# Optimization experiments

Measured on AMD Instinct MI355X. Metric: run time of the kernel, lower is better.

## Reference

```python
import jax, jax.numpy as jnp
import numpy as np

HIDDEN = 7168
NH = 32
DQ = 1536
DKV = 512
DH = 128   # up_projected_head_size
DR = 64    # rope_head_size
ROPE_BASE = 10000.0


def rms_norm(x, g):
    eps = jnp.finfo(x.dtype).eps
    var = jnp.mean(x * x, axis=-1, keepdims=True)
    return x * jax.lax.rsqrt(var + eps) * g


def apply_rope(x):
    # x: [B, H, S, D] -- rotate-half RoPE with cos/sin built as cat(freqs,freqs)
    S, D = x.shape[-2], x.shape[-1]
    inv_freq = 1.0 / (ROPE_BASE ** (jnp.arange(0, D, 2, dtype=jnp.float32) / D))
    t = jnp.arange(S, dtype=jnp.float32)
    freqs = jnp.outer(t, inv_freq)                 # [S, D/2]
    emb = jnp.concatenate([freqs, freqs], axis=-1)  # [S, D]
    cos, sin = jnp.cos(emb), jnp.sin(emb)
    x1, x2 = x[..., : D // 2], x[..., D // 2:]
    rotated = jnp.concatenate([-x2, x1], axis=-1)
    return x * cos + rotated * sin


def setup_inputs() -> dict:
    key = jax.random.key(0)
    ks = jax.random.split(key, 8)
    s = 0.02
    return {
        "hidden_states": jax.random.normal(ks[0], (1, 2048, HIDDEN), jnp.float32),
        "W_dq": jax.random.normal(ks[1], (HIDDEN, DQ), jnp.float32) * s,
        "g_q": jnp.ones((DQ,), jnp.float32),
        "W_uq": jax.random.normal(ks[2], (DQ, NH * (DH + DR)), jnp.float32) * s,
        "W_dkv": jax.random.normal(ks[3], (HIDDEN, DKV + DR), jnp.float32) * s,
        "g_kv": jnp.ones((DKV,), jnp.float32),
        "W_ukv": jax.random.normal(ks[4], (DKV, NH * 2 * DH), jnp.float32) * s,
        "W_o": jax.random.normal(ks[5], (NH * DH, HIDDEN), jnp.float32) * s,
    }


def reference(hidden_states, W_dq, g_q, W_uq, W_dkv, g_kv, W_ukv, W_o):
    B, S, _ = hidden_states.shape
    # Q path: down-proj -> RMSNorm -> up-proj -> split nope/rope parts
    c_q = hidden_states @ W_dq                                   # [B,S,DQ]
    qcr = (rms_norm(c_q, g_q) @ W_uq).reshape(B, S, NH, DH + DR)
    qcr = qcr.transpose(0, 2, 1, 3)                              # [B,NH,S,DH+DR]
    q_c, q_r = qcr[..., :DH], qcr[..., DH:]
    # KV path: joint down-proj for compressed latent + shared MQA rope key
    ckv_kr = hidden_states @ W_dkv                               # [B,S,DKV+DR]
    c_kv, k_r = ckv_kr[..., :DKV], ckv_kr[..., DKV:]
    k_r = k_r[:, None, :, :]                                     # [B,1,S,DR]
    kv = (rms_norm(c_kv, g_kv) @ W_ukv).reshape(B, S, NH, 2 * DH)
    kv = kv.transpose(0, 2, 1, 3)                                # [B,NH,S,2*DH]
    k_c, v = kv[..., :DH], kv[..., DH:]
    # partial RoPE
    q_r = apply_rope(q_r)
    k_r = apply_rope(k_r)
    q = jnp.concatenate([q_c, q_r], axis=-1)                     # [B,NH,S,DH+DR]
    k = jnp.concatenate([k_c, jnp.broadcast_to(k_r, (B, NH, S, DR))], axis=-1)
    # non-causal SDPA, scale = 1/sqrt(q head dim)
    scale = 1.0 / np.sqrt(DH + DR)
    scores = jnp.einsum("bhqd,bhkd->bhqk", q, k) * scale
    attn = jax.nn.softmax(scores, axis=-1)
    o = jnp.einsum("bhqk,bhkd->bhqd", attn, v)                   # [B,NH,S,DH]
    o = o.transpose(0, 2, 1, 3).reshape(B, S, NH * DH)
    return o @ W_o
```

## Files before the change

### kernel.cpp

```cpp
#include <hip/hip_runtime.h>
#include <hip/hip_bf16.h>
#include <math.h>

#define HIDDEN 7168
#define NH 32
#define DQ 1536
#define DKV 512
#define DH 128
#define DR 64
#define SEQ 2048
#define DKVP 640
#define NQKV 2176

typedef unsigned short u16;
typedef __bf16 bf16_t;
typedef bf16_t bf16x8 __attribute__((ext_vector_type(8)));
typedef float f32x4 __attribute__((ext_vector_type(4)));

__device__ __forceinline__ float bf2f(u16 h) {
    union { unsigned u; float f; } q; q.u = ((unsigned)h) << 16; return q.f;
}
__device__ __forceinline__ u16 f2bf(float x) {
    union { float f; unsigned u; } q; q.f = x;
    unsigned r = q.u + 0x7fffu + ((q.u >> 16) & 1u);
    return (u16)(r >> 16);
}

template <typename CT>
__global__ __launch_bounds__(256) void gemm_bt(
    const u16* __restrict__ A, const u16* __restrict__ B, CT* __restrict__ C,
    int K, int lda, int ldb, int ldc, long sA, long sB, long sC)
{
    __shared__ u16 As[128 * 32];
    __shared__ u16 Bs[128 * 32];
    A += (long)blockIdx.z * sA;
    B += (long)blockIdx.z * sB;
    C += (long)blockIdx.z * sC;

    const int t = threadIdx.x;
    const int w = t >> 6, lane = t & 63;
    const int lane15 = lane & 15, quad = lane >> 4;
    const int brow = blockIdx.y * 128, bcol = blockIdx.x * 128;
    const int wrow = (w >> 1) * 64, wcol = (w & 1) * 64;

    f32x4 acc[4][4] = {};

    for (int k0 = 0; k0 < K; k0 += 32) {
#pragma unroll
        for (int i = 0; i < 2; ++i) {
            int chunk = i * 256 + t;
            int row = chunk >> 2;
            int kc = (chunk & 3) * 8;
            const u16* ga = A + (long)(brow + row) * lda + k0 + kc;
            const u16* gb = B + (long)(bcol + row) * ldb + k0 + kc;
            u16* la = As + (i * 256 + w * 64) * 8;
            u16* lb = Bs + (i * 256 + w * 64) * 8;
            __builtin_amdgcn_global_load_lds(
                (const __attribute__((address_space(1))) void*)ga,
                (__attribute__((address_space(3))) void*)la, 16, 0, 0);
            __builtin_amdgcn_global_load_lds(
                (const __attribute__((address_space(1))) void*)gb,
                (__attribute__((address_space(3))) void*)lb, 16, 0, 0);
        }
        __syncthreads();

        bf16x8 af[4], bfr[4];
#pragma unroll
        for (int mi = 0; mi < 4; ++mi)
            af[mi] = *(const bf16x8*)(As + (wrow + mi * 16 + lane15) * 32 + quad * 8);
#pragma unroll
        for (int ni = 0; ni < 4; ++ni)
            bfr[ni] = *(const bf16x8*)(Bs + (wcol + ni * 16 + lane15) * 32 + quad * 8);
#pragma unroll
        for (int mi = 0; mi < 4; ++mi)
#pragma unroll
            for (int ni = 0; ni < 4; ++ni)
                acc[mi][ni] = __builtin_amdgcn_mfma_f32_16x16x32_bf16(
                    af[mi], bfr[ni], acc[mi][ni], 0, 0, 0);
        __syncthreads();
    }

#pragma unroll
    for (int mi = 0; mi < 4; ++mi) {
#pragma unroll
        for (int ni = 0; ni < 4; ++ni) {
            int r0 = brow + wrow + mi * 16 + quad * 4;
            int cc = bcol + wcol + ni * 16 + lane15;
#pragma unroll
            for (int r = 0; r < 4; ++r) {
                float v = acc[mi][ni][r];
                if constexpr (sizeof(CT) == 2) C[(long)(r0 + r) * ldc + cc] = f2bf(v);
                else                           C[(long)(r0 + r) * ldc + cc] = v;
            }
        }
    }
}

template <typename CT>
__global__ __launch_bounds__(512, 2) void gemm256(
    const u16* __restrict__ A, const u16* __restrict__ B, CT* __restrict__ C,
    int K, int lda, int ldb, int ldc, int nx)
{
    __shared__ u16 lds[4 * 16384];
    const int t = threadIdx.x;
    const int lane = t & 63;
    const int w = t >> 6;
    const int lane15 = lane & 15, quad = lane >> 4;
    const int wm = w >> 2, wn = w & 3;

    int nwg = gridDim.x, wg = blockIdx.x, tile = wg;
    if ((nwg & 7) == 0) { int q = nwg >> 3; tile = (wg & 7) * q + (wg >> 3); }
    const int bx = tile % nx, by = tile / nx;
    const long brow = (long)by * 256, bcol = (long)bx * 256;

    const u16* gsrc[4];
    int loff[4];
#pragma unroll
    for (int j = 0; j < 2; ++j) {
        int c = j * 512 + t;
        int row = c >> 2, k8 = (c & 3) * 8;
        gsrc[j]     = A + (brow + row) * lda + k8;
        gsrc[j + 2] = B + (bcol + row) * ldb + k8;
        loff[j]     = c * 8;
        loff[j + 2] = 8192 + c * 8;
    }

    const int NT = K >> 5;
    auto stage = [&](int tt) {
        u16* sb = lds + (tt & 3) * 16384;
        int ko = tt * 32;
#pragma unroll
        for (int j = 0; j < 4; ++j)
            __builtin_amdgcn_global_load_lds(
                (const __attribute__((address_space(1))) void*)(gsrc[j] + ko),
                (__attribute__((address_space(3))) void*)(sb + loff[j]), 16, 0, 0);
    };

    f32x4 acc[8][4] = {};
    const int aoff = (wm * 128 + lane15) * 32 + quad * 8;
    const int boff = 8192 + (wn * 64 + lane15) * 32 + quad * 8;

    stage(0); stage(1); stage(2);

    for (int T = 0; T < NT; ++T) {
        int rem = NT - 1 - T;
        if (rem >= 2)      asm volatile("s_waitcnt vmcnt(8)" ::: "memory");
        else if (rem == 1) asm volatile("s_waitcnt vmcnt(4)" ::: "memory");
        else               asm volatile("s_waitcnt vmcnt(0)" ::: "memory");
        __builtin_amdgcn_s_barrier();
        __builtin_amdgcn_sched_barrier(0);
        if (T + 3 < NT) stage(T + 3);

        const u16* sb = lds + (T & 3) * 16384;
        bf16x8 bfr[4], af[8];
#pragma unroll
        for (int ni = 0; ni < 4; ++ni)
            bfr[ni] = *(const bf16x8*)(sb + boff + ni * 512);
#pragma unroll
        for (int mi = 0; mi < 4; ++mi)
            af[mi] = *(const bf16x8*)(sb + aoff + mi * 512);
        __builtin_amdgcn_s_setprio(1);
#pragma unroll
        for (int mi = 0; mi < 4; ++mi)
#pragma unroll
            for (int ni = 0; ni < 4; ++ni)
                acc[mi][ni] = __builtin_amdgcn_mfma_f32_16x16x32_bf16(
                    af[mi], bfr[ni], acc[mi][ni], 0, 0, 0);
        __builtin_amdgcn_s_setprio(0);
#pragma unroll
        for (int mi = 4; mi < 8; ++mi)
            af[mi] = *(const bf16x8*)(sb + aoff + mi * 512);
        __builtin_amdgcn_s_setprio(1);
#pragma unroll
        for (int mi = 4; mi < 8; ++mi)
#pragma unroll
            for (int ni = 0; ni < 4; ++ni)
                acc[mi][ni] = __builtin_amdgcn_mfma_f32_16x16x32_bf16(
                    af[mi], bfr[ni], acc[mi][ni], 0, 0, 0);
        __builtin_amdgcn_s_setprio(0);
        asm volatile("s_waitcnt lgkmcnt(0)" ::: "memory");
        __builtin_amdgcn_sched_barrier(0);
    }

    const long crow0 = brow + wm * 128 + quad * 4;
    const long ccol0 = bcol + wn * 64 + lane15;
#pragma unroll
    for (int mi = 0; mi < 8; ++mi) {
#pragma unroll
        for (int ni = 0; ni < 4; ++ni) {
            long r0 = crow0 + mi * 16;
            long cc = ccol0 + ni * 16;
#pragma unroll
            for (int r = 0; r < 4; ++r) {
                float v = acc[mi][ni][r];
                if constexpr (sizeof(CT) == 2) C[(r0 + r) * ldc + cc] = f2bf(v);
                else                           C[(r0 + r) * ldc + cc] = v;
            }
        }
    }
}

__global__ __launch_bounds__(256, 2) void flash_attn(
    const u16* __restrict__ qb, const u16* __restrict__ kb,
    const u16* __restrict__ vT, u16* __restrict__ ob, float scale)
{
    __shared__ u16 Ks[64 * 200];
    __shared__ u16 Vs[128 * 72];
    __shared__ u16 Ps[4 * 32 * 72];

    const int t = threadIdx.x;
    const int w = t >> 6, lane = t & 63;
    const int lane15 = lane & 15, quad = lane >> 4;
    const int h = blockIdx.y;
    const int q0 = blockIdx.x * 128 + w * 32;
    u16* Psw = Ps + w * 32 * 72;

    bf16x8 Qf[2][6];
#pragma unroll
    for (int qt = 0; qt < 2; ++qt)
#pragma unroll
        for (int kc = 0; kc < 6; ++kc)
            Qf[qt][kc] = *(const bf16x8*)(
                qb + (long)(h * SEQ + q0 + qt * 16 + lane15) * 192 + kc * 32 + quad * 8);

    f32x4 O[8][2] = {};
    float mst[2] = { -3.0e38f, -3.0e38f }, lst[2] = { 0.f, 0.f };

    bf16x8 Kpf[6], Vpf[4];
    auto load_tiles = [&](int kt) {
#pragma unroll
        for (int i = 0; i < 6; ++i) {
            int chunk = i * 256 + t;
            int row = chunk / 24, c8 = (chunk % 24) * 8;
            Kpf[i] = *(const bf16x8*)(kb + (long)(h * SEQ + kt * 64 + row) * 192 + c8);
        }
#pragma unroll
        for (int i = 0; i < 4; ++i) {
            int chunk = i * 256 + t;
            int dh = chunk >> 3, c8 = (chunk & 7) * 8;
            Vpf[i] = *(const bf16x8*)(vT + (long)(h * 128 + dh) * SEQ + kt * 64 + c8);
        }
    };
    auto store_tiles = [&]() {
#pragma unroll
        for (int i = 0; i < 6; ++i) {
            int chunk = i * 256 + t;
            int row = chunk / 24, c8 = (chunk % 24) * 8;
            *(bf16x8*)(Ks + row * 200 + c8) = Kpf[i];
        }
#pragma unroll
        for (int i = 0; i < 4; ++i) {
            int chunk = i * 256 + t;
            int dh = chunk >> 3, c8 = (chunk & 7) * 8;
            *(bf16x8*)(Vs + dh * 72 + c8) = Vpf[i];
        }
    };

    load_tiles(0);
    store_tiles();
    __syncthreads();

    for (int kt = 0; kt < SEQ / 64; ++kt) {
        load_tiles(kt + 1 < SEQ / 64 ? kt + 1 : kt);

        f32x4 St[4][2] = {};
#pragma unroll
        for (int kc = 0; kc < 6; ++kc) {
            bf16x8 Kf[4];
#pragma unroll
            for (int k4 = 0; k4 < 4; ++k4)
                Kf[k4] = *(const bf16x8*)(Ks + (k4 * 16 + lane15) * 200 + kc * 32 + quad * 8);
#pragma unroll
            for (int k4 = 0; k4 < 4; ++k4)
#pragma unroll
                for (int qt = 0; qt < 2; ++qt)
                    St[k4][qt] = __builtin_amdgcn_mfma_f32_16x16x32_bf16(
                        Kf[k4], Qf[qt][kc], St[k4][qt], 0, 0, 0);
        }

#pragma unroll
        for (int qt = 0; qt < 2; ++qt) {
            float rm = St[0][qt][0];
#pragma unroll
            for (int k4 = 0; k4 < 4; ++k4)
#pragma unroll
                for (int r = 0; r < 4; ++r) rm = fmaxf(rm, St[k4][qt][r]);
            rm = fmaxf(rm, __shfl_xor(rm, 16, 64));
            rm = fmaxf(rm, __shfl_xor(rm, 32, 64));
            rm *= scale;
            float mnew = fmaxf(mst[qt], rm);
            float alpha = __expf(mst[qt] - mnew);
            mst[qt] = mnew;
            float rs = 0.f;
#pragma unroll
            for (int k4 = 0; k4 < 4; ++k4)
#pragma unroll
                for (int r = 0; r < 4; ++r) {
                    float pv = __expf(St[k4][qt][r] * scale - mnew);
                    St[k4][qt][r] = pv; rs += pv;
                }
            rs += __shfl_xor(rs, 16, 64);
            rs += __shfl_xor(rs, 32, 64);
            lst[qt] = lst[qt] * alpha + rs;
#pragma unroll
            for (int dt = 0; dt < 8; ++dt)
#pragma unroll
                for (int r = 0; r < 4; ++r) O[dt][qt][r] *= alpha;
        }

#pragma unroll
        for (int qt = 0; qt < 2; ++qt)
#pragma unroll
            for (int k4 = 0; k4 < 4; ++k4) {
                ushort4 pk;
                pk.x = f2bf(St[k4][qt][0]); pk.y = f2bf(St[k4][qt][1]);
                pk.z = f2bf(St[k4][qt][2]); pk.w = f2bf(St[k4][qt][3]);
                *(ushort4*)(Psw + (qt * 16 + lane15) * 72 + k4 * 16 + quad * 4) = pk;
            }

#pragma unroll
        for (int kc2 = 0; kc2 < 2; ++kc2) {
            bf16x8 Pf[2], Vf[8];
#pragma unroll
            for (int qt = 0; qt < 2; ++qt)
                Pf[qt] = *(const bf16x8*)(Psw + (qt * 16 + lane15) * 72 + kc2 * 32 + quad * 8);
#pragma unroll
            for (int dt = 0; dt < 8; ++dt)
                Vf[dt] = *(const bf16x8*)(Vs + (dt * 16 + lane15) * 72 + kc2 * 32 + quad * 8);
#pragma unroll
            for (int dt = 0; dt < 8; ++dt)
#pragma unroll
                for (int qt = 0; qt < 2; ++qt)
                    O[dt][qt] = __builtin_amdgcn_mfma_f32_16x16x32_bf16(
                        Vf[dt], Pf[qt], O[dt][qt], 0, 0, 0);
        }
        __syncthreads();
        store_tiles();
        __syncthreads();
    }

#pragma unroll
    for (int qt = 0; qt < 2; ++qt) {
        float inv = 1.f / lst[qt];
        int s = q0 + qt * 16 + lane15;
#pragma unroll
        for (int dt = 0; dt < 8; ++dt) {
            ushort4 ov;
            ov.x = f2bf(O[dt][qt][0] * inv); ov.y = f2bf(O[dt][qt][1] * inv);
            ov.z = f2bf(O[dt][qt][2] * inv); ov.w = f2bf(O[dt][qt][3] * inv);
            *(ushort4*)(ob + (long)s * 4096 + h * 128 + dt * 16 + quad * 4) = ov;
        }
    }
}

__global__ void cast_bf16_k(const float* __restrict__ in, u16* __restrict__ out, long n)
{
    long i = ((long)blockIdx.x * 256 + threadIdx.x) * 4;
    if (i >= n) return;
    float4 v = *(const float4*)(in + i);
    ushort4 o;
    o.x = f2bf(v.x); o.y = f2bf(v.y); o.z = f2bf(v.z); o.w = f2bf(v.w);
    *(ushort4*)(out + i) = o;
}

__global__ void transpose_cast(const float* __restrict__ in, u16* __restrict__ out,
                               int K, int N, int Npad)
{
    __shared__ float tile[32][33];
    int n0 = blockIdx.x * 32, k0 = blockIdx.y * 32;
    int tx = threadIdx.x, ty = threadIdx.y;
#pragma unroll
    for (int i = 0; i < 32; i += 8) {
        int k = k0 + ty + i, n = n0 + tx;
        tile[ty + i][tx] = (n < N) ? in[(long)k * N + n] : 0.f;
    }
    __syncthreads();
#pragma unroll
    for (int i = 0; i < 32; i += 8) {
        int n = n0 + ty + i, k = k0 + tx;
        out[(long)n * K + k] = f2bf(tile[tx][ty + i]);
    }
}

__global__ __launch_bounds__(256) void rmsnorm_k(
    const u16* __restrict__ in, const float* __restrict__ g,
    u16* __restrict__ out, int C, int ldin)
{
    const int row = blockIdx.x;
    const u16* x = in + (long)row * ldin;
    float ss = 0.f;
    for (int c = threadIdx.x; c < C; c += 256) { float v = bf2f(x[c]); ss += v * v; }
#pragma unroll
    for (int off = 32; off; off >>= 1) ss += __shfl_down(ss, off, 64);
    __shared__ float red[4];
    if ((threadIdx.x & 63) == 0) red[threadIdx.x >> 6] = ss;
    __syncthreads();
    float tot = red[0] + red[1] + red[2] + red[3];
    float r = rsqrtf(tot / (float)C + 1.1920929e-07f);
    for (int c = threadIdx.x; c < C; c += 256)
        out[(long)row * C + c] = f2bf(bf2f(x[c]) * r * g[c]);
}

__global__ void rope_tab_k(float* __restrict__ ct, float* __restrict__ st)
{
    int idx = blockIdx.x * 256 + threadIdx.x;
    int s = idx >> 5, j = idx & 31;
    float invf = powf(10000.f, -(float)(2 * j) / 64.f);
    float fr = (float)s * invf;
    float sn, cs; sincosf(fr, &sn, &cs);
    ct[idx] = cs; st[idx] = sn;
}

__device__ __forceinline__ float rope_val(const u16* src, int i, int s,
                                          const float* ct, const float* st)
{
    int j = i & 31;
    float cs = ct[s * 32 + j], sn = st[s * 32 + j];
    float x = bf2f(src[i]);
    float xo = (i < 32) ? bf2f(src[i + 32]) : bf2f(src[i - 32]);
    return (i < 32) ? (x * cs - xo * sn) : (x * cs + xo * sn);
}

__global__ void build_q_k(const u16* __restrict__ qcr, u16* __restrict__ q,
                          const float* __restrict__ ct, const float* __restrict__ st)
{
    int s = blockIdx.x, h = blockIdx.y, d = threadIdx.x;
    const u16* src = qcr + ((long)s * NH + h) * 192;
    float val = (d < 128) ? bf2f(src[d]) : rope_val(src + 128, d - 128, s, ct, st);
    q[((long)h * SEQ + s) * 192 + d] = f2bf(val);
}

__global__ void build_k_k(const u16* __restrict__ kv, const u16* __restrict__ ropebuf,
                          int ldrope, u16* __restrict__ kbuf,
                          const float* __restrict__ ct, const float* __restrict__ st)
{
    int s = blockIdx.x, h = blockIdx.y, d = threadIdx.x;
    float val = (d < 128) ? bf2f(kv[(long)s * 8192 + h * 256 + d])
                          : rope_val(ropebuf + (long)s * ldrope, d - 128, s, ct, st);
    kbuf[((long)h * SEQ + s) * 192 + d] = f2bf(val);
}

__global__ void build_vT_k(const u16* __restrict__ kv, u16* __restrict__ vT)
{
    __shared__ u16 tile[32][33];
    int s0 = blockIdx.x * 32, d0 = blockIdx.y * 32, h = blockIdx.z;
    int tx = threadIdx.x, ty = threadIdx.y;
#pragma unroll
    for (int i = 0; i < 32; i += 8)
        tile[ty + i][tx] = kv[(long)(s0 + ty + i) * 8192 + h * 256 + 128 + d0 + tx];
    __syncthreads();
#pragma unroll
    for (int i = 0; i < 32; i += 8)
        vT[((long)h * 128 + d0 + ty + i) * SEQ + s0 + tx] = tile[tx][ty + i];
}

extern "C" void kernel_launch(void* const* d_in, const int* in_sizes, int n_in,
                              void* d_out, int out_size, void* d_ws, size_t ws_size,
                              hipStream_t stream)
{
    const float* hidden = (const float*)d_in[0];
    const float* W_dq   = (const float*)d_in[1];
    const float* g_q    = (const float*)d_in[2];
    const float* W_uq   = (const float*)d_in[3];
    const float* W_dkv  = (const float*)d_in[4];
    const float* g_kv   = (const float*)d_in[5];
    const float* W_ukv  = (const float*)d_in[6];
    const float* W_o    = (const float*)d_in[7];
    float* out = (float*)d_out;

    char* p = (char*)d_ws;
    auto alloc = [&](size_t bytes) {
        char* r = p; p += (bytes + 255) & ~(size_t)255; return r;
    };
    u16* hbf   = (u16*)alloc((size_t)SEQ * HIDDEN * 2);
    u16* WTqkv = (u16*)alloc((size_t)NQKV * HIDDEN * 2);
    u16* WTuq  = (u16*)alloc((size_t)6144 * DQ * 2);
    u16* WTukv = (u16*)alloc((size_t)8192 * DKV * 2);
    u16* WTo   = (u16*)alloc((size_t)HIDDEN * 4096 * 2);
    u16* cqc   = (u16*)alloc((size_t)SEQ * NQKV * 2);
    u16* nq    = (u16*)alloc((size_t)SEQ * DQ * 2);
    u16* qcr   = (u16*)alloc((size_t)SEQ * 6144 * 2);
    u16* nkv   = (u16*)alloc((size_t)SEQ * DKV * 2);
    u16* kvb   = (u16*)alloc((size_t)SEQ * 8192 * 2);
    u16* qb    = (u16*)alloc((size_t)NH * SEQ * 192 * 2);
    u16* kb    = (u16*)alloc((size_t)NH * SEQ * 192 * 2);
    u16* vT    = (u16*)alloc((size_t)NH * 128 * SEQ * 2);
    u16* ob    = (u16*)alloc((size_t)SEQ * 4096 * 2);
    float* ct  = (float*)alloc((size_t)SEQ * 32 * 4);
    float* st  = (float*)alloc((size_t)SEQ * 32 * 4);
    (void)in_sizes; (void)n_in; (void)out_size; (void)ws_size;

    rope_tab_k<<<(SEQ * 32) / 256, 256, 0, stream>>>(ct, st);
    cast_bf16_k<<<((long)SEQ * HIDDEN) / 1024, 256, 0, stream>>>(hidden, hbf, (long)SEQ * HIDDEN);
    transpose_cast<<<dim3(DQ / 32, HIDDEN / 32), dim3(32, 8), 0, stream>>>(W_dq, WTqkv, HIDDEN, DQ, DQ);
    transpose_cast<<<dim3(DKVP / 32, HIDDEN / 32), dim3(32, 8), 0, stream>>>(
        W_dkv, WTqkv + (size_t)DQ * HIDDEN, HIDDEN, 576, DKVP);
    transpose_cast<<<dim3(6144 / 32, DQ / 32), dim3(32, 8), 0, stream>>>(W_uq, WTuq, DQ, 6144, 6144);
    transpose_cast<<<dim3(8192 / 32, DKV / 32), dim3(32, 8), 0, stream>>>(W_ukv, WTukv, DKV, 8192, 8192);
    transpose_cast<<<dim3(HIDDEN / 32, 4096 / 32), dim3(32, 8), 0, stream>>>(W_o, WTo, 4096, HIDDEN, HIDDEN);

    gemm_bt<u16><<<dim3(NQKV / 128, SEQ / 128), 256, 0, stream>>>(
        hbf, WTqkv, cqc, HIDDEN, HIDDEN, HIDDEN, NQKV, 0, 0, 0);
    rmsnorm_k<<<SEQ, 256, 0, stream>>>(cqc, g_q, nq, DQ, NQKV);
    rmsnorm_k<<<SEQ, 256, 0, stream>>>(cqc + DQ, g_kv, nkv, DKV, NQKV);

    gemm256<u16><<<dim3((SEQ / 256) * (6144 / 256)), 512, 0, stream>>>(
        nq, WTuq, qcr, DQ, DQ, DQ, 6144, 6144 / 256);
    gemm256<u16><<<dim3((SEQ / 256) * (8192 / 256)), 512, 0, stream>>>(
        nkv, WTukv, kvb, DKV, DKV, DKV, 8192, 8192 / 256);

    build_q_k<<<dim3(SEQ, NH), 192, 0, stream>>>(qcr, qb, ct, st);
    build_k_k<<<dim3(SEQ, NH), 192, 0, stream>>>(kvb, cqc + DQ + DKV, NQKV, kb, ct, st);
    build_vT_k<<<dim3(SEQ / 32, 4, NH), dim3(32, 8), 0, stream>>>(kvb, vT);

    const float scale = 0.07216878364870322f;
    flash_attn<<<dim3(SEQ / 128, NH), 256, 0, stream>>>(qb, kb, vT, ob, scale);

    gemm256<float><<<dim3((SEQ / 256) * (HIDDEN / 256)), 512, 0, stream>>>(
        ob, WTo, out, 4096, 4096, 4096, HIDDEN, HIDDEN / 256);
}
```

Measured before the change: 887.8 us.

## Split-K the QKV down-projection and split gemm256 prefetch into halves

The first down-projection GEMM (K=7168) is split four ways along K using the grid z dimension. Each split writes fp32 partials into a reused scratch buffer, and a new reduce kernel sums them and converts the result to bf16. This gives the GEMM more workgroups, since it previously had only 17x16 tiles. In gemm256, the next-stage prefetch is issued in two halves around an extra barrier, spreading global-to-LDS loads across the MFMA phases. The cost is extra fp32 partial traffic, one more kernel launch, and an added barrier per iteration.

Result: faster. 849.8 us (-4.3%).

```diff
diff --git a/kernel.cpp b/kernel.cpp
--- a/kernel.cpp
+++ b/kernel.cpp
@@ -11,6 +11,7 @@
 #define SEQ 2048
 #define DKVP 640
 #define NQKV 2176
+#define SK 4
 
 typedef unsigned short u16;
 typedef __bf16 bf16_t;
@@ -96,6 +97,23 @@
     }
 }
 
+__global__ __launch_bounds__(256) void reduce_sk_k(
+    const float* __restrict__ part, u16* __restrict__ out, long n, long ps)
+{
+    long i = ((long)blockIdx.x * 256 + threadIdx.x) * 4;
+    if (i >= n) return;
+    float4 s0 = *(const float4*)(part + i);
+    float4 s1 = *(const float4*)(part + ps + i);
+    float4 s2 = *(const float4*)(part + 2 * ps + i);
+    float4 s3 = *(const float4*)(part + 3 * ps + i);
+    ushort4 o;
+    o.x = f2bf(s0.x + s1.x + s2.x + s3.x);
+    o.y = f2bf(s0.y + s1.y + s2.y + s3.y);
+    o.z = f2bf(s0.z + s1.z + s2.z + s3.z);
+    o.w = f2bf(s0.w + s1.w + s2.w + s3.w);
+    *(ushort4*)(out + i) = o;
+}
+
 template <typename CT>
 __global__ __launch_bounds__(512, 2) void gemm256(
     const u16* __restrict__ A, const u16* __restrict__ B, CT* __restrict__ C,
@@ -126,11 +144,11 @@
     }
 
     const int NT = K >> 5;
-    auto stage = [&](int tt) {
+    auto stage2 = [&](int tt, int h) {
         u16* sb = lds + (tt & 3) * 16384;
         int ko = tt * 32;
 #pragma unroll
-        for (int j = 0; j < 4; ++j)
+        for (int j = h * 2; j < h * 2 + 2; ++j)
             __builtin_amdgcn_global_load_lds(
                 (const __attribute__((address_space(1))) void*)(gsrc[j] + ko),
                 (__attribute__((address_space(3))) void*)(sb + loff[j]), 16, 0, 0);
@@ -140,7 +158,9 @@
     const int aoff = (wm * 128 + lane15) * 32 + quad * 8;
     const int boff = 8192 + (wn * 64 + lane15) * 32 + quad * 8;
 
-    stage(0); stage(1); stage(2);
+    stage2(0, 0); stage2(0, 1);
+    stage2(1, 0); stage2(1, 1);
+    stage2(2, 0); stage2(2, 1);
 
     for (int T = 0; T < NT; ++T) {
         int rem = NT - 1 - T;
@@ -149,9 +169,11 @@
         else               asm volatile("s_waitcnt vmcnt(0)" ::: "memory");
         __builtin_amdgcn_s_barrier();
         __builtin_amdgcn_sched_barrier(0);
-        if (T + 3 < NT) stage(T + 3);
 
         const u16* sb = lds + (T & 3) * 16384;
+        const bool pf = (T + 3 < NT);
+
+        if (pf) stage2(T + 3, 0);
         bf16x8 bfr[4], af[8];
 #pragma unroll
         for (int ni = 0; ni < 4; ++ni)
@@ -167,6 +189,11 @@
                 acc[mi][ni] = __builtin_amdgcn_mfma_f32_16x16x32_bf16(
                     af[mi], bfr[ni], acc[mi][ni], 0, 0, 0);
         __builtin_amdgcn_s_setprio(0);
+
+        __builtin_amdgcn_s_barrier();
+        __builtin_amdgcn_sched_barrier(0);
+
+        if (pf) stage2(T + 3, 1);
 #pragma unroll
         for (int mi = 4; mi < 8; ++mi)
             af[mi] = *(const bf16x8*)(sb + aoff + mi * 512);
@@ -490,6 +517,8 @@
     float* st  = (float*)alloc((size_t)SEQ * 32 * 4);
     (void)in_sizes; (void)n_in; (void)out_size; (void)ws_size;
 
+    float* part = (float*)qcr;
+
     rope_tab_k<<<(SEQ * 32) / 256, 256, 0, stream>>>(ct, st);
     cast_bf16_k<<<((long)SEQ * HIDDEN) / 1024, 256, 0, stream>>>(hidden, hbf, (long)SEQ * HIDDEN);
     transpose_cast<<<dim3(DQ / 32, HIDDEN / 32), dim3(32, 8), 0, stream>>>(W_dq, WTqkv, HIDDEN, DQ, DQ);
@@ -499,8 +528,12 @@
     transpose_cast<<<dim3(8192 / 32, DKV / 32), dim3(32, 8), 0, stream>>>(W_ukv, WTukv, DKV, 8192, 8192);
     transpose_cast<<<dim3(HIDDEN / 32, 4096 / 32), dim3(32, 8), 0, stream>>>(W_o, WTo, 4096, HIDDEN, HIDDEN);
 
-    gemm_bt<u16><<<dim3(NQKV / 128, SEQ / 128), 256, 0, stream>>>(
-        hbf, WTqkv, cqc, HIDDEN, HIDDEN, HIDDEN, NQKV, 0, 0, 0);
+    gemm_bt<float><<<dim3(NQKV / 128, SEQ / 128, SK), 256, 0, stream>>>(
+        hbf, WTqkv, part, HIDDEN / SK, HIDDEN, HIDDEN, NQKV,
+        HIDDEN / SK, HIDDEN / SK, (long)SEQ * NQKV);
+    reduce_sk_k<<<((long)SEQ * NQKV) / 1024, 256, 0, stream>>>(
+        part, cqc, (long)SEQ * NQKV, (long)SEQ * NQKV);
+
     rmsnorm_k<<<SEQ, 256, 0, stream>>>(cqc, g_q, nq, DQ, NQKV);
     rmsnorm_k<<<SEQ, 256, 0, stream>>>(cqc + DQ, g_kv, nkv, DKV, NQKV);
 
```
